# Kernel optimization log

Hardware: AMD Instinct MI355X
Metric: run time of the kernel (lower is better)

Reference implementation:

```python
import jax, jax.numpy as jnp
import numpy as np

N, IN_DIM, OUT_DIM = 8192, 512, 256
ALPHA = 0.2  # LeakyReLU negative slope
MASK_VAL = -9e15


def setup_inputs() -> dict:
    key = jax.random.key(0)
    k1, k2, k3, k4 = jax.random.split(key, 4)
    inp = jax.random.normal(k1, (N, IN_DIM), dtype=jnp.float32)
    adj = jax.random.randint(k2, (N, N), 0, 2, dtype=jnp.int32)
    # xavier-ish scaled params
    weight = jax.random.normal(k3, (IN_DIM, OUT_DIM), dtype=jnp.float32) * (2.0 / (IN_DIM + OUT_DIM)) ** 0.5
    a = jax.random.normal(k4, (2 * OUT_DIM, 1), dtype=jnp.float32) * (2.0 / (2 * OUT_DIM + 1)) ** 0.5
    return {"input": inp, "adj": adj, "weight": weight, "a": a}


def reference(input, adj, weight, a):
    Wh = input @ weight                        # [N, D_out]
    Wh1 = Wh @ a[:OUT_DIM, :]                  # [N, 1]
    Wh2 = Wh @ a[OUT_DIM:, :]                  # [N, 1]
    e = Wh1 + Wh2.T                            # [N, N] broadcast additive score
    e = jnp.where(e > 0, e, ALPHA * e)         # LeakyReLU
    e = jnp.where(adj > 0, e, MASK_VAL)        # adjacency mask
    attention = jax.nn.softmax(e, axis=-1)     # [N, N]
    # dropout p=0.0 -> identity
    out = attention @ Wh                       # [N, D_out]
    return jax.nn.elu(out)
```

## Files before the change

kernel.cpp:

```cpp
#include <hip/hip_runtime.h>
#include <hip/hip_bf16.h>
#include <stdint.h>

#define NN 8192
#define DIN 512
#define DOUT 256
#define NSPLIT 8
#define STRIP (NN / NSPLIT)
#define NSTEP (STRIP / 32)
#define LOG2E 1.4426950408889634f

typedef short short8 __attribute__((ext_vector_type(8)));
typedef float floatx4 __attribute__((ext_vector_type(4)));

__device__ __forceinline__ unsigned short f2bf_rne(float x) {
  unsigned u = __float_as_uint(x);
  u += 0x7fffu + ((u >> 16) & 1u);
  return (unsigned short)(u >> 16);
}

__device__ __forceinline__ unsigned cvt_pk_bf16(float lo, float hi) {
  unsigned r;
  asm("v_cvt_pk_bf16_f32 %0, %1, %2" : "=v"(r) : "v"(lo), "v"(hi));
  return r;
}

__global__ __launch_bounds__(256) void kt_transpose(const float* __restrict__ Wg,
                                                    unsigned short* __restrict__ WT) {
  __shared__ unsigned short sm[32][33];
  int tid = threadIdx.x;
  int bk = blockIdx.x >> 3;
  int bn = blockIdx.x & 7;
  int k0 = bk * 32, n0 = bn * 32;
  int r = tid >> 3, c4 = (tid & 7) * 4;
  const float* src = Wg + (size_t)(k0 + r) * DOUT + n0 + c4;
#pragma unroll
  for (int x = 0; x < 4; ++x) sm[r][c4 + x] = f2bf_rne(src[x]);
  __syncthreads();
  unsigned short* dst = WT + (size_t)(n0 + r) * DIN + k0 + c4;
#pragma unroll
  for (int x = 0; x < 4; ++x) dst[x] = sm[c4 + x][r];
}

__global__ __launch_bounds__(256) void kt_cvtx(const float* __restrict__ X,
                                               unsigned short* __restrict__ Xb) {
  int g = blockIdx.x * 256 + threadIdx.x;
  const float4* p = (const float4*)(X + (size_t)g * 8);
  float4 a = p[0], b = p[1];
  union { unsigned u[4]; short8 s8; } r;
  r.u[0] = cvt_pk_bf16(a.x, a.y);
  r.u[1] = cvt_pk_bf16(a.z, a.w);
  r.u[2] = cvt_pk_bf16(b.x, b.y);
  r.u[3] = cvt_pk_bf16(b.z, b.w);
  *(short8*)(Xb + (size_t)g * 8) = r.s8;
}

__global__ __launch_bounds__(256, 2) void kt_gemm1(const unsigned short* __restrict__ Xb,
                                                   const unsigned short* __restrict__ WT,
                                                   const float* __restrict__ Ab,
                                                   unsigned short* __restrict__ WhT,
                                                   float* __restrict__ Wh1,
                                                   float* __restrict__ Wh2) {
  __shared__ __align__(16) unsigned short xs[64 * DIN];
  int tid = threadIdx.x;
  int w = tid >> 6, lane = tid & 63;
  int col = lane & 15, q = lane >> 4;
  int ib = blockIdx.x & 127;
  int db = blockIdx.x >> 7;
  int i0 = ib * 64;

  int sr = tid >> 2, sc = tid & 3, sxor = sr & 7;
  const unsigned short* gX = Xb + (size_t)(i0 + sr) * DIN + sc * 8;
  unsigned short* lX = xs + sr * DIN;
  short8 stg[8];
#pragma unroll
  for (int n = 0; n < 8; ++n) stg[n] = *(const short8*)(gX + n * 32);
#pragma unroll
  for (int n = 0; n < 8; ++n) {
    int l = sc + n * 4;
    *(short8*)(lX + ((l ^ sxor) * 8)) = stg[n];
  }
#pragma unroll
  for (int n = 8; n < 16; ++n) stg[n - 8] = *(const short8*)(gX + n * 32);
#pragma unroll
  for (int n = 8; n < 16; ++n) {
    int l = sc + n * 4;
    *(short8*)(lX + ((l ^ sxor) * 8)) = stg[n - 8];
  }

  int drow = db * 64 + w * 16 + col;
  const unsigned short* abase = WT + (size_t)drow * DIN + q * 8;
  short8 af[16];
#pragma unroll
  for (int s = 0; s < 16; ++s) af[s] = *(const short8*)(abase + s * 32);

  __syncthreads();

  floatx4 acc[4];
#pragma unroll
  for (int t = 0; t < 4; ++t) acc[t] = (floatx4)(0.0f);
  int cx = col & 7;
#pragma unroll
  for (int s = 0; s < 16; ++s) {
#pragma unroll
    for (int t = 0; t < 4; ++t) {
      short8 bf = *(const short8*)(xs + (t * 16 + col) * DIN + (((s * 4 + q) ^ cx) * 8));
      acc[t] = __builtin_amdgcn_mfma_f32_16x16x32_bf16(af[s], bf, acc[t], 0, 0, 0);
    }
  }

  int dq = db * 64 + w * 16 + q * 4;
  float a1v[4], a2v[4];
#pragma unroll
  for (int r = 0; r < 4; ++r) {
    a1v[r] = Ab[dq + r] * LOG2E;
    a2v[r] = Ab[DOUT + dq + r] * LOG2E;
  }
#pragma unroll
  for (int t = 0; t < 4; ++t) {
    floatx4 v = acc[t];
    int icol = i0 + t * 16 + col;
#pragma unroll
    for (int r = 0; r < 4; ++r) WhT[(size_t)(dq + r) * NN + icol] = f2bf_rne(v[r]);
    float p1 = v[0] * a1v[0] + v[1] * a1v[1] + v[2] * a1v[2] + v[3] * a1v[3];
    float p2 = v[0] * a2v[0] + v[1] * a2v[1] + v[2] * a2v[2] + v[3] * a2v[3];
    p1 += __shfl_xor(p1, 16);
    p1 += __shfl_xor(p1, 32);
    p2 += __shfl_xor(p2, 16);
    p2 += __shfl_xor(p2, 32);
    if (q == 0) {
      atomicAdd(&Wh1[icol], p1);
      atomicAdd(&Wh2[icol], p2);
    }
  }
}

__device__ __forceinline__ short8 build_a(int4 pa, int4 pb, float wh1, floatx4 w2a,
                                          floatx4 w2b, float& lsum) {
  int av[8] = {pa.x, pa.y, pa.z, pa.w, pb.x, pb.y, pb.z, pb.w};
  float w2[8] = {w2a[0], w2a[1], w2a[2], w2a[3], w2b[0], w2b[1], w2b[2], w2b[3]};
  float wv[8];
#pragma unroll
  for (int e = 0; e < 8; ++e) {
    float sc = wh1 + w2[e];
    sc = fmaxf(sc, 0.2f * sc);
    float ex = __builtin_amdgcn_exp2f(sc);
    wv[e] = (av[e] != 0) ? ex : 0.0f;
  }
  union { unsigned u[4]; short8 s8; } r;
#pragma unroll
  for (int p = 0; p < 4; ++p) {
    unsigned pk = cvt_pk_bf16(wv[2 * p], wv[2 * p + 1]);
    r.u[p] = pk;
    lsum += __uint_as_float(pk << 16) + __uint_as_float(pk & 0xffff0000u);
  }
  return r.s8;
}

__global__ __launch_bounds__(256, 2) void kt_attn(const int* __restrict__ adj,
                                                  const unsigned short* __restrict__ WhT,
                                                  const float* __restrict__ Wh1,
                                                  const float* __restrict__ Wh2,
                                                  float* __restrict__ accg,
                                                  float* __restrict__ lg) {
  __shared__ __align__(16) unsigned short tileB[2][DOUT * 32];
  int tid = threadIdx.x;
  int w = tid >> 6, lane = tid & 63;
  int col = lane & 15, q = lane >> 4;
  int s = blockIdx.x & (NSPLIT - 1);
  int ib = blockIdx.x >> 3;
  int i0 = ib * 128;
  int jb = s * STRIP;
  int r0 = i0 + w * 32 + col;
  float wh1r0 = Wh1[r0];
  float wh1r1 = Wh1[r0 + 16];
  int fsw = (tid >> 1) & 3;
  const unsigned short* gsrc = WhT + (size_t)tid * NN + jb;
  unsigned short* lrow0 = &tileB[0][tid * 32];
  int fc = (col >> 1) & 3;
  const unsigned short* bb0 = &tileB[0][col * 32 + ((q ^ fc) * 8)];
  const int* aptr0 = adj + ((size_t)r0 << 13) + jb + q * 8;
  const int* aptr1 = adj + ((size_t)(r0 + 16) << 13) + jb + q * 8;
  const float* wp = Wh2 + jb + q * 8;
  floatx4 acc0[16], acc1[16];
#pragma unroll
  for (int t = 0; t < 16; ++t) {
    acc0[t] = (floatx4)(0.0f);
    acc1[t] = (floatx4)(0.0f);
  }
  float lp0 = 0.f, lp1 = 0.f;
  short8 st[4];
#pragma unroll
  for (int m = 0; m < 4; ++m) st[m] = *(const short8*)(gsrc + m * 8);
  int4 a0a = *(const int4*)aptr0;
  int4 a0b = *(const int4*)(aptr0 + 4);
  int4 a1a = *(const int4*)aptr1;
  int4 a1b = *(const int4*)(aptr1 + 4);
  floatx4 w2a = *(const floatx4*)wp;
  floatx4 w2b = *(const floatx4*)(wp + 4);
#pragma unroll 1
  for (int k = 0; k < NSTEP; ++k) {
    int bsel = (k & 1) * (DOUT * 32);
    unsigned short* lw = lrow0 + bsel;
#pragma unroll
    for (int m = 0; m < 4; ++m) *(short8*)(lw + ((m ^ fsw) * 8)) = st[m];
    if (k + 1 < NSTEP) {
      const unsigned short* gs = gsrc + (size_t)(k + 1) * 32;
#pragma unroll
      for (int m = 0; m < 4; ++m) st[m] = *(const short8*)(gs + m * 8);
    }
    asm volatile("s_waitcnt lgkmcnt(0)\ns_barrier" ::: "memory");
    short8 af0 = build_a(a0a, a0b, wh1r0, w2a, w2b, lp0);
    short8 af1 = build_a(a1a, a1b, wh1r1, w2a, w2b, lp1);
    if (k + 1 < NSTEP) {
      int jn = (k + 1) * 32;
      a0a = *(const int4*)(aptr0 + jn);
      a0b = *(const int4*)(aptr0 + jn + 4);
      a1a = *(const int4*)(aptr1 + jn);
      a1b = *(const int4*)(aptr1 + jn + 4);
      w2a = *(const floatx4*)(wp + jn);
      w2b = *(const floatx4*)(wp + jn + 4);
    }
#pragma unroll
    for (int h = 0; h < 4; ++h) {
      short8 bf[4];
#pragma unroll
      for (int t = 0; t < 4; ++t) bf[t] = *(const short8*)(bb0 + bsel + (h * 4 + t) * 512);
#pragma unroll
      for (int t = 0; t < 4; ++t) {
        acc0[h * 4 + t] =
            __builtin_amdgcn_mfma_f32_16x16x32_bf16(af0, bf[t], acc0[h * 4 + t], 0, 0, 0);
        acc1[h * 4 + t] =
            __builtin_amdgcn_mfma_f32_16x16x32_bf16(af1, bf[t], acc1[h * 4 + t], 0, 0, 0);
      }
    }
  }
  lp0 += __shfl_xor(lp0, 16);
  lp0 += __shfl_xor(lp0, 32);
  lp1 += __shfl_xor(lp1, 16);
  lp1 += __shfl_xor(lp1, 32);
  if (lane < 16) {
    atomicAdd(&lg[i0 + w * 32 + lane], lp0);
    atomicAdd(&lg[i0 + w * 32 + 16 + lane], lp1);
  }
#pragma unroll
  for (int T = 0; T < 16; ++T) {
    floatx4 v0 = acc0[T];
    floatx4 v1 = acc1[T];
    int dcol = T * 16 + col;
    int irow0 = i0 + w * 32 + q * 4;
#pragma unroll
    for (int r = 0; r < 4; ++r) atomicAdd(&accg[(size_t)(irow0 + r) * DOUT + dcol], v0[r]);
#pragma unroll
    for (int r = 0; r < 4; ++r)
      atomicAdd(&accg[(size_t)(irow0 + 16 + r) * DOUT + dcol], v1[r]);
  }
}

__global__ __launch_bounds__(256) void kt_merge(const float* __restrict__ accg,
                                                const float* __restrict__ lg,
                                                float* __restrict__ out) {
  int g = blockIdx.x * 256 + threadIdx.x;
  int i = g >> 6;
  float inv = 1.0f / lg[i];
  float4 v = *(const float4*)(accg + (size_t)g * 4);
  float o[4] = {v.x * inv, v.y * inv, v.z * inv, v.w * inv};
#pragma unroll
  for (int r = 0; r < 4; ++r) o[r] = o[r] > 0.f ? o[r] : (__expf(o[r]) - 1.f);
  *(float4*)(out + (size_t)g * 4) = make_float4(o[0], o[1], o[2], o[3]);
}

extern "C" void kernel_launch(void* const* d_in, const int* in_sizes, int n_in,
                              void* d_out, int out_size, void* d_ws, size_t ws_size,
                              hipStream_t stream) {
  const float* X = (const float*)d_in[0];
  const int* adj = (const int*)d_in[1];
  const float* Wg = (const float*)d_in[2];
  const float* Ab = (const float*)d_in[3];
  float* out = (float*)d_out;

  char* ws = (char*)d_ws;
  float* accg = (float*)ws;
  unsigned short* Xb = (unsigned short*)ws;
  size_t off = (size_t)NN * DOUT * 4;
  float* lg = (float*)(ws + off);
  off += (size_t)NN * 4;
  float* Wh1 = (float*)(ws + off);
  off += (size_t)NN * 4;
  float* Wh2 = (float*)(ws + off);
  off += (size_t)NN * 4;
  unsigned short* WT = (unsigned short*)(ws + off);
  off += (size_t)DOUT * DIN * 2;
  unsigned short* WhT = (unsigned short*)(ws + off);
  off += (size_t)DOUT * NN * 2;

  hipMemsetAsync(Wh1, 0, (size_t)NN * 8, stream);
  kt_cvtx<<<2048, 256, 0, stream>>>(X, Xb);
  kt_transpose<<<128, 256, 0, stream>>>(Wg, WT);
  kt_gemm1<<<512, 256, 0, stream>>>(Xb, WT, Ab, WhT, Wh1, Wh2);
  hipMemsetAsync(ws, 0, (size_t)NN * DOUT * 4 + (size_t)NN * 4, stream);
  kt_attn<<<(NN / 128) * NSPLIT, 256, 0, stream>>>(adj, WhT, Wh1, Wh2, accg, lg);
  kt_merge<<<2048, 256, 0, stream>>>(accg, lg, out);
}
```

Measured before the change: 461.0 us.

## Preload adjacency strip as bitmasks and block WhT into contiguous 32-column tiles

The attention kernel now reads its whole 128x1024 adjacency strip up front with coalesced int4 loads and packs it into per-row 32-bit masks in shared memory. The main loop then reads one mask word per row per step instead of doing scattered int loads. The first GEMM writes Wh transposed in a blocked layout ([N/32][DOUT][32]), so each K-step tile of B is one contiguous 16KB chunk instead of 256 strided rows. This trades some extra shared memory and an upfront serialized adjacency read (less overlap with the MFMA work) for better coalescing and fewer in-loop global loads.

After: 504.2 us. 1.09x slower.

```diff
diff --git a/kernel.cpp b/kernel.cpp
--- a/kernel.cpp
+++ b/kernel.cpp
@@ -58,7 +58,7 @@
 __global__ __launch_bounds__(256, 2) void kt_gemm1(const unsigned short* __restrict__ Xb,
                                                    const unsigned short* __restrict__ WT,
                                                    const float* __restrict__ Ab,
-                                                   unsigned short* __restrict__ WhT,
+                                                   unsigned short* __restrict__ WhTb,
                                                    float* __restrict__ Wh1,
                                                    float* __restrict__ Wh2) {
   __shared__ __align__(16) unsigned short xs[64 * DIN];
@@ -121,7 +121,8 @@
     floatx4 v = acc[t];
     int icol = i0 + t * 16 + col;
 #pragma unroll
-    for (int r = 0; r < 4; ++r) WhT[(size_t)(dq + r) * NN + icol] = f2bf_rne(v[r]);
+    for (int r = 0; r < 4; ++r)
+      WhTb[((size_t)(icol >> 5) * DOUT + (dq + r)) * 32 + (icol & 31)] = f2bf_rne(v[r]);
     float p1 = v[0] * a1v[0] + v[1] * a1v[1] + v[2] * a1v[2] + v[3] * a1v[3];
     float p2 = v[0] * a2v[0] + v[1] * a2v[1] + v[2] * a2v[2] + v[3] * a2v[3];
     p1 += __shfl_xor(p1, 16);
@@ -135,9 +136,8 @@
   }
 }
 
-__device__ __forceinline__ short8 build_a(int4 pa, int4 pb, float wh1, floatx4 w2a,
+__device__ __forceinline__ short8 build_a(unsigned bq, float wh1, floatx4 w2a,
                                           floatx4 w2b, float& lsum) {
-  int av[8] = {pa.x, pa.y, pa.z, pa.w, pb.x, pb.y, pb.z, pb.w};
   float w2[8] = {w2a[0], w2a[1], w2a[2], w2a[3], w2b[0], w2b[1], w2b[2], w2b[3]};
   float wv[8];
 #pragma unroll
@@ -145,7 +145,7 @@
     float sc = wh1 + w2[e];
     sc = fmaxf(sc, 0.2f * sc);
     float ex = __builtin_amdgcn_exp2f(sc);
-    wv[e] = (av[e] != 0) ? ex : 0.0f;
+    wv[e] = ((bq >> e) & 1u) ? ex : 0.0f;
   }
   union { unsigned u[4]; short8 s8; } r;
 #pragma unroll
@@ -158,12 +158,13 @@
 }
 
 __global__ __launch_bounds__(256, 2) void kt_attn(const int* __restrict__ adj,
-                                                  const unsigned short* __restrict__ WhT,
+                                                  const unsigned short* __restrict__ WhTb,
                                                   const float* __restrict__ Wh1,
                                                   const float* __restrict__ Wh2,
                                                   float* __restrict__ accg,
                                                   float* __restrict__ lg) {
   __shared__ __align__(16) unsigned short tileB[2][DOUT * 32];
+  __shared__ unsigned masks[128][33];
   int tid = threadIdx.x;
   int w = tid >> 6, lane = tid & 63;
   int col = lane & 15, q = lane >> 4;
@@ -171,17 +172,38 @@
   int ib = blockIdx.x >> 3;
   int i0 = ib * 128;
   int jb = s * STRIP;
+
+#pragma unroll 2
+  for (int rr = 0; rr < 32; ++rr) {
+    int row = w * 32 + rr;
+    const int* rp = adj + (size_t)(i0 + row) * NN + jb;
+#pragma unroll
+    for (int n = 0; n < 4; ++n) {
+      int4 v = *(const int4*)(rp + n * 256 + lane * 4);
+      unsigned word = ((unsigned)(v.x & 1) | ((unsigned)(v.y & 1) << 1) |
+                       ((unsigned)(v.z & 1) << 2) | ((unsigned)(v.w & 1) << 3))
+                      << ((lane & 7) * 4);
+      word |= __shfl_xor(word, 1);
+      word |= __shfl_xor(word, 2);
+      word |= __shfl_xor(word, 4);
+      if ((lane & 7) == 0) masks[row][n * 8 + (lane >> 3)] = word;
+    }
+  }
+
   int r0 = i0 + w * 32 + col;
   float wh1r0 = Wh1[r0];
   float wh1r1 = Wh1[r0 + 16];
-  int fsw = (tid >> 1) & 3;
-  const unsigned short* gsrc = WhT + (size_t)tid * NN + jb;
-  unsigned short* lrow0 = &tileB[0][tid * 32];
+  int qs = q * 8;
+  int rl0 = w * 32 + col, rl1 = rl0 + 16;
+
+  const unsigned short* gW = WhTb + (size_t)(s * 32) * 8192 + tid * 8;
+  int wswz = ((tid & 3) ^ ((tid >> 3) & 3)) * 8;
+  unsigned short* lw0 = &tileB[0][(tid >> 2) * 32 + wswz];
   int fc = (col >> 1) & 3;
   const unsigned short* bb0 = &tileB[0][col * 32 + ((q ^ fc) * 8)];
-  const int* aptr0 = adj + ((size_t)r0 << 13) + jb + q * 8;
-  const int* aptr1 = adj + ((size_t)(r0 + 16) << 13) + jb + q * 8;
-  const float* wp = Wh2 + jb + q * 8;
+
+  const float* wp = Wh2 + jb + qs;
+
   floatx4 acc0[16], acc1[16];
 #pragma unroll
   for (int t = 0; t < 16; ++t) {
@@ -189,37 +211,37 @@
     acc1[t] = (floatx4)(0.0f);
   }
   float lp0 = 0.f, lp1 = 0.f;
+
   short8 st[4];
 #pragma unroll
-  for (int m = 0; m < 4; ++m) st[m] = *(const short8*)(gsrc + m * 8);
-  int4 a0a = *(const int4*)aptr0;
-  int4 a0b = *(const int4*)(aptr0 + 4);
-  int4 a1a = *(const int4*)aptr1;
-  int4 a1b = *(const int4*)(aptr1 + 4);
+  for (int m = 0; m < 4; ++m) st[m] = *(const short8*)(gW + m * 2048);
+
+  asm volatile("s_waitcnt lgkmcnt(0)\ns_barrier" ::: "memory");
+
+  unsigned mw0 = masks[rl0][0], mw1 = masks[rl1][0];
   floatx4 w2a = *(const floatx4*)wp;
   floatx4 w2b = *(const floatx4*)(wp + 4);
+
 #pragma unroll 1
   for (int k = 0; k < NSTEP; ++k) {
     int bsel = (k & 1) * (DOUT * 32);
-    unsigned short* lw = lrow0 + bsel;
-#pragma unroll
-    for (int m = 0; m < 4; ++m) *(short8*)(lw + ((m ^ fsw) * 8)) = st[m];
+    unsigned short* lw = lw0 + bsel;
+#pragma unroll
+    for (int m = 0; m < 4; ++m) *(short8*)(lw + m * 2048) = st[m];
     if (k + 1 < NSTEP) {
-      const unsigned short* gs = gsrc + (size_t)(k + 1) * 32;
-#pragma unroll
-      for (int m = 0; m < 4; ++m) st[m] = *(const short8*)(gs + m * 8);
+      const unsigned short* gs = gW + (size_t)(k + 1) * 8192;
+#pragma unroll
+      for (int m = 0; m < 4; ++m) st[m] = *(const short8*)(gs + m * 2048);
     }
     asm volatile("s_waitcnt lgkmcnt(0)\ns_barrier" ::: "memory");
-    short8 af0 = build_a(a0a, a0b, wh1r0, w2a, w2b, lp0);
-    short8 af1 = build_a(a1a, a1b, wh1r1, w2a, w2b, lp1);
+    short8 af0 = build_a(mw0 >> qs, wh1r0, w2a, w2b, lp0);
+    short8 af1 = build_a(mw1 >> qs, wh1r1, w2a, w2b, lp1);
     if (k + 1 < NSTEP) {
-      int jn = (k + 1) * 32;
-      a0a = *(const int4*)(aptr0 + jn);
-      a0b = *(const int4*)(aptr0 + jn + 4);
-      a1a = *(const int4*)(aptr1 + jn);
-      a1b = *(const int4*)(aptr1 + jn + 4);
-      w2a = *(const floatx4*)(wp + jn);
-      w2b = *(const floatx4*)(wp + jn + 4);
+      mw0 = masks[rl0][k + 1];
+      mw1 = masks[rl1][k + 1];
+      const float* wn = wp + (k + 1) * 32;
+      w2a = *(const floatx4*)wn;
+      w2b = *(const floatx4*)(wn + 4);
     }
 #pragma unroll
     for (int h = 0; h < 4; ++h) {
@@ -235,6 +257,7 @@
       }
     }
   }
+
   lp0 += __shfl_xor(lp0, 16);
   lp0 += __shfl_xor(lp0, 32);
   lp1 += __shfl_xor(lp1, 16);
@@ -291,14 +314,14 @@
   off += (size_t)NN * 4;
   unsigned short* WT = (unsigned short*)(ws + off);
   off += (size_t)DOUT * DIN * 2;
-  unsigned short* WhT = (unsigned short*)(ws + off);
+  unsigned short* WhTb = (unsigned short*)(ws + off);
   off += (size_t)DOUT * NN * 2;
 
   hipMemsetAsync(Wh1, 0, (size_t)NN * 8, stream);
   kt_cvtx<<<2048, 256, 0, stream>>>(X, Xb);
   kt_transpose<<<128, 256, 0, stream>>>(Wg, WT);
-  kt_gemm1<<<512, 256, 0, stream>>>(Xb, WT, Ab, WhT, Wh1, Wh2);
+  kt_gemm1<<<512, 256, 0, stream>>>(Xb, WT, Ab, WhTb, Wh1, Wh2);
   hipMemsetAsync(ws, 0, (size_t)NN * DOUT * 4 + (size_t)NN * 4, stream);
-  kt_attn<<<(NN / 128) * NSPLIT, 256, 0, stream>>>(adj, WhT, Wh1, Wh2, accg, lg);
+  kt_attn<<<(NN / 128) * NSPLIT, 256, 0, stream>>>(adj, WhTb, Wh1, Wh2, accg, lg);
   kt_merge<<<2048, 256, 0, stream>>>(accg, lg, out);
 }
```

## Double KV block to 64 columns per step and stage Wh2 strip in LDS

Applied to the files above, without the earlier changes.

Each main-loop iteration now processes 64 key columns in two 32-wide halves, halving the number of barriers and LDS double-buffer swaps per strip. The B tile becomes 64 wide with an 8-way XOR swizzle, and the Wh2 strip is loaded once into shared memory rather than fetched from global each step. This raises register pressure (twice the adjacency prefetch and staging registers) and LDS usage, which may reduce occupancy under launch_bounds(256,2).

Result: no change. 455.0 us (-1.3%).

```diff
diff --git a/kernel.cpp b/kernel.cpp
--- a/kernel.cpp
+++ b/kernel.cpp
@@ -7,7 +7,8 @@
 #define DOUT 256
 #define NSPLIT 8
 #define STRIP (NN / NSPLIT)
-#define NSTEP (STRIP / 32)
+#define KVBLK 64
+#define NSTEP (STRIP / KVBLK)
 #define LOG2E 1.4426950408889634f
 
 typedef short short8 __attribute__((ext_vector_type(8)));
@@ -163,7 +164,8 @@
                                                   const float* __restrict__ Wh2,
                                                   float* __restrict__ accg,
                                                   float* __restrict__ lg) {
-  __shared__ __align__(16) unsigned short tileB[2][DOUT * 32];
+  __shared__ __align__(16) unsigned short tileB[2][DOUT * KVBLK];
+  __shared__ __align__(16) float wh2s[STRIP];
   int tid = threadIdx.x;
   int w = tid >> 6, lane = tid & 63;
   int col = lane & 15, q = lane >> 4;
@@ -171,17 +173,25 @@
   int ib = blockIdx.x >> 3;
   int i0 = ib * 128;
   int jb = s * STRIP;
+
+  ((float4*)wh2s)[tid] = ((const float4*)(Wh2 + jb))[tid];
+
   int r0 = i0 + w * 32 + col;
   float wh1r0 = Wh1[r0];
   float wh1r1 = Wh1[r0 + 16];
-  int fsw = (tid >> 1) & 3;
+
+  int sw = tid & 7;
   const unsigned short* gsrc = WhT + (size_t)tid * NN + jb;
-  unsigned short* lrow0 = &tileB[0][tid * 32];
-  int fc = (col >> 1) & 3;
-  const unsigned short* bb0 = &tileB[0][col * 32 + ((q ^ fc) * 8)];
+  unsigned short* lrow0 = &tileB[0][tid * KVBLK];
+
+  int ck = col & 7;
+  int off0 = col * KVBLK + ((q ^ ck) * 8);
+  int off1 = col * KVBLK + (((4 + q) ^ ck) * 8);
+  const unsigned short* tb0 = &tileB[0][0];
+
   const int* aptr0 = adj + ((size_t)r0 << 13) + jb + q * 8;
   const int* aptr1 = adj + ((size_t)(r0 + 16) << 13) + jb + q * 8;
-  const float* wp = Wh2 + jb + q * 8;
+
   floatx4 acc0[16], acc1[16];
 #pragma unroll
   for (int t = 0; t < 16; ++t) {
@@ -189,52 +199,88 @@
     acc1[t] = (floatx4)(0.0f);
   }
   float lp0 = 0.f, lp1 = 0.f;
-  short8 st[4];
-#pragma unroll
-  for (int m = 0; m < 4; ++m) st[m] = *(const short8*)(gsrc + m * 8);
-  int4 a0a = *(const int4*)aptr0;
-  int4 a0b = *(const int4*)(aptr0 + 4);
-  int4 a1a = *(const int4*)aptr1;
-  int4 a1b = *(const int4*)(aptr1 + 4);
-  floatx4 w2a = *(const floatx4*)wp;
-  floatx4 w2b = *(const floatx4*)(wp + 4);
+
+  short8 st[8];
+#pragma unroll
+  for (int n = 0; n < 8; ++n) st[n] = *(const short8*)(gsrc + n * 8);
+  int4 aA0a = *(const int4*)aptr0;
+  int4 aA0b = *(const int4*)(aptr0 + 4);
+  int4 aA1a = *(const int4*)aptr1;
+  int4 aA1b = *(const int4*)(aptr1 + 4);
+  int4 aB0a = *(const int4*)(aptr0 + 32);
+  int4 aB0b = *(const int4*)(aptr0 + 36);
+  int4 aB1a = *(const int4*)(aptr1 + 32);
+  int4 aB1b = *(const int4*)(aptr1 + 36);
+
 #pragma unroll 1
   for (int k = 0; k < NSTEP; ++k) {
-    int bsel = (k & 1) * (DOUT * 32);
+    int bsel = (k & 1) * (DOUT * KVBLK);
     unsigned short* lw = lrow0 + bsel;
 #pragma unroll
-    for (int m = 0; m < 4; ++m) *(short8*)(lw + ((m ^ fsw) * 8)) = st[m];
+    for (int n = 0; n < 8; ++n) *(short8*)(lw + ((n ^ sw) * 8)) = st[n];
     if (k + 1 < NSTEP) {
-      const unsigned short* gs = gsrc + (size_t)(k + 1) * 32;
-#pragma unroll
-      for (int m = 0; m < 4; ++m) st[m] = *(const short8*)(gs + m * 8);
+      const unsigned short* gs = gsrc + (size_t)(k + 1) * KVBLK;
+#pragma unroll
+      for (int n = 0; n < 8; ++n) st[n] = *(const short8*)(gs + n * 8);
     }
     asm volatile("s_waitcnt lgkmcnt(0)\ns_barrier" ::: "memory");
-    short8 af0 = build_a(a0a, a0b, wh1r0, w2a, w2b, lp0);
-    short8 af1 = build_a(a1a, a1b, wh1r1, w2a, w2b, lp1);
-    if (k + 1 < NSTEP) {
-      int jn = (k + 1) * 32;
-      a0a = *(const int4*)(aptr0 + jn);
-      a0b = *(const int4*)(aptr0 + jn + 4);
-      a1a = *(const int4*)(aptr1 + jn);
-      a1b = *(const int4*)(aptr1 + jn + 4);
-      w2a = *(const floatx4*)(wp + jn);
-      w2b = *(const floatx4*)(wp + jn + 4);
-    }
-#pragma unroll
-    for (int h = 0; h < 4; ++h) {
-      short8 bf[4];
-#pragma unroll
-      for (int t = 0; t < 4; ++t) bf[t] = *(const short8*)(bb0 + bsel + (h * 4 + t) * 512);
-#pragma unroll
-      for (int t = 0; t < 4; ++t) {
-        acc0[h * 4 + t] =
-            __builtin_amdgcn_mfma_f32_16x16x32_bf16(af0, bf[t], acc0[h * 4 + t], 0, 0, 0);
-        acc1[h * 4 + t] =
-            __builtin_amdgcn_mfma_f32_16x16x32_bf16(af1, bf[t], acc1[h * 4 + t], 0, 0, 0);
+    int jl = k * KVBLK;
+    {
+      floatx4 w2a = *(const floatx4*)&wh2s[jl + q * 8];
+      floatx4 w2b = *(const floatx4*)&wh2s[jl + q * 8 + 4];
+      short8 af0 = build_a(aA0a, aA0b, wh1r0, w2a, w2b, lp0);
+      short8 af1 = build_a(aA1a, aA1b, wh1r1, w2a, w2b, lp1);
+      if (k + 1 < NSTEP) {
+        int jn = (k + 1) * KVBLK;
+        aA0a = *(const int4*)(aptr0 + jn);
+        aA0b = *(const int4*)(aptr0 + jn + 4);
+        aA1a = *(const int4*)(aptr1 + jn);
+        aA1b = *(const int4*)(aptr1 + jn + 4);
       }
-    }
-  }
+      const unsigned short* br = tb0 + bsel + off0;
+#pragma unroll
+      for (int h = 0; h < 4; ++h) {
+        short8 bf[4];
+#pragma unroll
+        for (int t = 0; t < 4; ++t) bf[t] = *(const short8*)(br + (h * 4 + t) * 1024);
+#pragma unroll
+        for (int t = 0; t < 4; ++t) {
+          acc0[h * 4 + t] =
+              __builtin_amdgcn_mfma_f32_16x16x32_bf16(af0, bf[t], acc0[h * 4 + t], 0, 0, 0);
+          acc1[h * 4 + t] =
+              __builtin_amdgcn_mfma_f32_16x16x32_bf16(af1, bf[t], acc1[h * 4 + t], 0, 0, 0);
+        }
+      }
+    }
+    {
+      floatx4 w2a = *(const floatx4*)&wh2s[jl + 32 + q * 8];
+      floatx4 w2b = *(const floatx4*)&wh2s[jl + 32 + q * 8 + 4];
+      short8 ag0 = build_a(aB0a, aB0b, wh1r0, w2a, w2b, lp0);
+      short8 ag1 = build_a(aB1a, aB1b, wh1r1, w2a, w2b, lp1);
+      if (k + 1 < NSTEP) {
+        int jn = (k + 1) * KVBLK + 32;
+        aB0a = *(const int4*)(aptr0 + jn);
+        aB0b = *(const int4*)(aptr0 + jn + 4);
+        aB1a = *(const int4*)(aptr1 + jn);
+        aB1b = *(const int4*)(aptr1 + jn + 4);
+      }
+      const unsigned short* br = tb0 + bsel + off1;
+#pragma unroll
+      for (int h = 0; h < 4; ++h) {
+        short8 bf[4];
+#pragma unroll
+        for (int t = 0; t < 4; ++t) bf[t] = *(const short8*)(br + (h * 4 + t) * 1024);
+#pragma unroll
+        for (int t = 0; t < 4; ++t) {
+          acc0[h * 4 + t] =
+              __builtin_amdgcn_mfma_f32_16x16x32_bf16(ag0, bf[t], acc0[h * 4 + t], 0, 0, 0);
+          acc1[h * 4 + t] =
+              __builtin_amdgcn_mfma_f32_16x16x32_bf16(ag1, bf[t], acc1[h * 4 + t], 0, 0, 0);
+        }
+      }
+    }
+  }
+
   lp0 += __shfl_xor(lp0, 16);
   lp0 += __shfl_xor(lp0, 32);
   lp1 += __shfl_xor(lp1, 16);
```
